# Kernel tuning notes

Measured on AMD Instinct MI355X. Metric: run time of the kernel, lower is better.

## Reference

```python
import jax, jax.numpy as jnp
import numpy as np

B, L, S, D, H, TOPK = 8, 2048, 1000, 1024, 8, 10
E = D // H  # d_keys = 128


def setup_inputs() -> dict:
    key = jax.random.key(0)
    ks = jax.random.split(key, 8)
    s = 1.0 / np.sqrt(D)
    return {
        "target_embedding": jax.random.normal(ks[0], (B, L, D), dtype=jnp.float32),
        "source_embedding": jax.random.normal(ks[1], (S, D), dtype=jnp.float32),
        "Wq": jax.random.normal(ks[2], (D, D), dtype=jnp.float32) * s,
        "bq": jnp.zeros((D,), dtype=jnp.float32),
        "Wk": jax.random.normal(ks[3], (D, D), dtype=jnp.float32) * s,
        "bk": jnp.zeros((D,), dtype=jnp.float32),
        "Wo": jax.random.normal(ks[4], (D, D), dtype=jnp.float32) * s,
        "bo": jnp.zeros((D,), dtype=jnp.float32),
        "data_id": 0,
    }


def reference(target_embedding, source_embedding, Wq, bq, Wk, bk, Wo, bo, data_id):
    # data_id is unused by the original module's math.
    b, l, d = target_embedding.shape
    h, e, topk = H, E, TOPK
    scale = 1.0 / np.sqrt(e)

    q = (target_embedding @ Wq + bq).reshape(b, l, h, e)   # [B,L,H,E]
    k = (source_embedding @ Wk + bk).reshape(-1, h, e)      # [S,H,E]

    scores = jnp.einsum('blhe,she->bhls', q, k)             # [B,H,L,S]
    A = jax.nn.softmax(scale * scores, axis=-1)             # dropout is eval-mode identity
    tmps = A.sum(axis=2)                                    # [B,H,S] head-wise column mass
    _, idxs = jax.lax.top_k(tmps, topk)                     # [B,H,topk]

    kh = jnp.transpose(k, (1, 0, 2))                        # [H,S,E]
    # gather per (batch, head) the topk source key vectors
    tok = kh[jnp.arange(h)[None, :, None], idxs, :]         # [B,H,topk,E]
    tok = jnp.transpose(tok, (0, 2, 1, 3)).reshape(b, topk, h * e)  # [B,topk,D]
    return tok @ Wo + bo                                    # [B,topk,D]
```

## Files before the change

### kernel.cpp

```cpp
#include <hip/hip_runtime.h>
#include <hip/hip_bf16.h>
#include <math.h>

constexpr int B_ = 8;
constexpr int L_ = 2048;
constexpr int S_ = 1000;
constexpr int D_ = 1024;
constexpr int H_ = 8;
constexpr int E_ = 128;
constexpr int TOPK_ = 10;
constexpr float SCALE_LOG2E_ = 0.12751744f;

typedef __attribute__((ext_vector_type(8))) short short8;
typedef __attribute__((ext_vector_type(4))) float f32x4;

__device__ inline unsigned short f2bf(float x) {
    unsigned u = __float_as_uint(x);
    unsigned r = (u + 0x7fffu + ((u >> 16) & 1u)) >> 16;
    return (unsigned short)r;
}
__device__ inline float bf2f(unsigned short s) {
    return __uint_as_float(((unsigned)s) << 16);
}

__device__ __forceinline__ float fexp2(float x) {
#if __has_builtin(__builtin_amdgcn_exp2f)
    return __builtin_amdgcn_exp2f(x);
#else
    return __expf(x * 0.69314718056f);
#endif
}

typedef __attribute__((address_space(1))) const unsigned int gas_u32;
typedef __attribute__((address_space(3))) unsigned int las_u32;
__device__ __forceinline__ void gload_lds16(const void* g, void* l) {
    __builtin_amdgcn_global_load_lds((gas_u32*)g, (las_u32*)l, 16, 0, 0);
}

__global__ __launch_bounds__(256) void gemm_bias_kernel(
    const float* __restrict__ A, const float* __restrict__ Bm,
    const float* __restrict__ bias, float* __restrict__ C,
    int M, int N, int Kd)
{
    __shared__ float As[16][65];
    __shared__ float Bs[16][68];

    const int t  = threadIdx.x;
    const int tx = t & 15;
    const int ty = t >> 4;
    const int m0 = blockIdx.y * 64;
    const int n0 = blockIdx.x * 64;

    float acc[4][4];
#pragma unroll
    for (int i = 0; i < 4; ++i)
#pragma unroll
        for (int j = 0; j < 4; ++j) acc[i][j] = 0.f;

    for (int k0 = 0; k0 < Kd; k0 += 16) {
        {
            const int row = t >> 2;
            const int c4  = (t & 3) * 4;
            float4 v = {0.f, 0.f, 0.f, 0.f};
            if (m0 + row < M)
                v = *(const float4*)&A[(size_t)(m0 + row) * Kd + k0 + c4];
            As[c4 + 0][row] = v.x;
            As[c4 + 1][row] = v.y;
            As[c4 + 2][row] = v.z;
            As[c4 + 3][row] = v.w;
        }
        {
            const int row = t >> 4;
            const int c4  = (t & 15) * 4;
            float4 v = *(const float4*)&Bm[(size_t)(k0 + row) * N + n0 + c4];
            *(float4*)&Bs[row][c4] = v;
        }
        __syncthreads();
#pragma unroll
        for (int k = 0; k < 16; ++k) {
            float a[4], b[4];
#pragma unroll
            for (int i = 0; i < 4; ++i) a[i] = As[k][ty * 4 + i];
            float4 bv = *(const float4*)&Bs[k][tx * 4];
            b[0] = bv.x; b[1] = bv.y; b[2] = bv.z; b[3] = bv.w;
#pragma unroll
            for (int i = 0; i < 4; ++i)
#pragma unroll
                for (int j = 0; j < 4; ++j) acc[i][j] += a[i] * b[j];
        }
        __syncthreads();
    }

#pragma unroll
    for (int i = 0; i < 4; ++i) {
        const int row = m0 + ty * 4 + i;
        if (row < M) {
#pragma unroll
            for (int j = 0; j < 4; ++j) {
                const int col = n0 + tx * 4 + j;
                C[(size_t)row * N + col] = acc[i][j] + bias[col];
            }
        }
    }
}

__global__ __launch_bounds__(256) void splitWT_kernel(
    const float* __restrict__ W,
    unsigned short* __restrict__ WTh, unsigned short* __restrict__ WTl)
{
    __shared__ __attribute__((aligned(16))) float tile[64][68];
    const int t  = threadIdx.x;
    const int k0 = blockIdx.y * 64, n0 = blockIdx.x * 64;
#pragma unroll
    for (int it = 0; it < 4; ++it) {
        int id = it * 256 + t;
        int r = id >> 4, c = id & 15;
        *(float4*)&tile[r][c * 4] = *(const float4*)&W[(size_t)(k0 + r) * D_ + n0 + c * 4];
    }
    __syncthreads();
#pragma unroll
    for (int it = 0; it < 4; ++it) {
        int id = it * 256 + t;
        int n = id >> 4, c = id & 15;
        unsigned short hs[4], ls[4];
#pragma unroll
        for (int i = 0; i < 4; ++i) {
            float x = tile[c * 4 + i][n];
            hs[i] = f2bf(x);
            ls[i] = f2bf(x - bf2f(hs[i]));
        }
        size_t o = (size_t)(n0 + n) * D_ + k0 + c * 4;
        uint2 uh; uh.x = (unsigned)hs[0] | ((unsigned)hs[1] << 16);
                  uh.y = (unsigned)hs[2] | ((unsigned)hs[3] << 16);
        uint2 ul; ul.x = (unsigned)ls[0] | ((unsigned)ls[1] << 16);
                  ul.y = (unsigned)ls[2] | ((unsigned)ls[3] << 16);
        *(uint2*)&WTh[o] = uh;
        *(uint2*)&WTl[o] = ul;
    }
}

__global__ __launch_bounds__(256) void split_src_kernel(
    const float* __restrict__ src,
    unsigned short* __restrict__ Sh, unsigned short* __restrict__ Sl)
{
    int idx  = blockIdx.x * 256 + threadIdx.x;
    int base = idx * 4;
    int row  = base >> 10;
    float4 v = {0.f, 0.f, 0.f, 0.f};
    if (row < S_) v = *(const float4*)&src[base];
    float xs[4] = {v.x, v.y, v.z, v.w};
    unsigned short hs[4], ls[4];
#pragma unroll
    for (int i = 0; i < 4; ++i) {
        hs[i] = f2bf(xs[i]);
        ls[i] = f2bf(xs[i] - bf2f(hs[i]));
    }
    uint2 uh; uh.x = (unsigned)hs[0] | ((unsigned)hs[1] << 16);
              uh.y = (unsigned)hs[2] | ((unsigned)hs[3] << 16);
    uint2 ul; ul.x = (unsigned)ls[0] | ((unsigned)ls[1] << 16);
              ul.y = (unsigned)ls[2] | ((unsigned)ls[3] << 16);
    *(uint2*)&Sh[base] = uh;
    *(uint2*)&Sl[base] = ul;
}

__global__ __launch_bounds__(256, 2) void kproj_kernel(
    const unsigned short* __restrict__ Sh, const unsigned short* __restrict__ Sl,
    const unsigned short* __restrict__ WkTh, const unsigned short* __restrict__ WkTl,
    const float* __restrict__ bk,
    float* __restrict__ Kbuf,
    unsigned short* __restrict__ Kh, unsigned short* __restrict__ Kl)
{
    __shared__ __attribute__((aligned(16))) unsigned short Ah[128 * 64];
    __shared__ __attribute__((aligned(16))) unsigned short Al[128 * 64];
    __shared__ __attribute__((aligned(16))) unsigned short Bh[128 * 64];
    __shared__ __attribute__((aligned(16))) unsigned short Bl[128 * 64];

    const int t    = threadIdx.x;
    const int lane = t & 63, w = t >> 6;
    const int mb   = blockIdx.x >> 3;
    const int n0   = (blockIdx.x & 7) * 128;

    f32x4 acc[2][8];
#pragma unroll
    for (int m = 0; m < 2; ++m)
#pragma unroll
        for (int n = 0; n < 8; ++n) acc[m][n] = (f32x4){0.f, 0.f, 0.f, 0.f};

    for (int k0 = 0; k0 < D_; k0 += 64) {
        __syncthreads();
#pragma unroll
        for (int it = 0; it < 4; ++it) {
            int r = it * 32 + (t >> 3), c = t & 7;
            size_t gofs = (size_t)r * D_ + k0 + ((c ^ (r & 7)) << 3);
            int db = it * 4096 + t * 16;
            gload_lds16(&Sh[(size_t)(mb * 128) * D_ + gofs], (char*)Ah + db);
            gload_lds16(&Sl[(size_t)(mb * 128) * D_ + gofs], (char*)Al + db);
            gload_lds16(&WkTh[(size_t)n0 * D_ + gofs], (char*)Bh + db);
            gload_lds16(&WkTl[(size_t)n0 * D_ + gofs], (char*)Bl + db);
        }
        __syncthreads();

#pragma unroll
        for (int ki = 0; ki < 2; ++ki) {
            short8 ah[2], al[2];
#pragma unroll
            for (int m = 0; m < 2; ++m) {
                int r = w * 32 + m * 16 + (lane & 15);
                int slot = ki * 4 + (lane >> 4);
                int lofs = r * 64 + ((slot ^ (r & 7)) << 3);
                ah[m] = *(short8*)&Ah[lofs];
                al[m] = *(short8*)&Al[lofs];
            }
#pragma unroll
            for (int n = 0; n < 8; ++n) {
                int nn = n * 16 + (lane & 15);
                int slot = ki * 4 + (lane >> 4);
                int lofs = nn * 64 + ((slot ^ (nn & 7)) << 3);
                short8 bh = *(short8*)&Bh[lofs];
                short8 bl = *(short8*)&Bl[lofs];
#pragma unroll
                for (int m = 0; m < 2; ++m) {
                    acc[m][n] = __builtin_amdgcn_mfma_f32_16x16x32_bf16(ah[m], bh, acc[m][n], 0, 0, 0);
                    acc[m][n] = __builtin_amdgcn_mfma_f32_16x16x32_bf16(ah[m], bl, acc[m][n], 0, 0, 0);
                    acc[m][n] = __builtin_amdgcn_mfma_f32_16x16x32_bf16(al[m], bh, acc[m][n], 0, 0, 0);
                }
            }
        }
    }

#pragma unroll
    for (int n = 0; n < 8; ++n) {
        int col = n0 + n * 16 + (lane & 15);
        float bkv = bk[col];
#pragma unroll
        for (int m = 0; m < 2; ++m) {
            int rbase = mb * 128 + w * 32 + m * 16 + ((lane >> 4) << 2);
#pragma unroll
            for (int r = 0; r < 4; ++r) {
                int row = rbase + r;
                unsigned short hh = 0, ll = 0;
                if (row < S_) {
                    float kv = acc[m][n][r] + bkv;
                    Kbuf[(size_t)row * D_ + col] = kv;
                    hh = f2bf(kv);
                    ll = f2bf(kv - bf2f(hh));
                }
                Kh[(size_t)row * D_ + col] = hh;
                Kl[(size_t)row * D_ + col] = ll;
            }
        }
    }
}

__global__ __launch_bounds__(256, 3) void qproj_kernel(
    const float* __restrict__ tgt,
    const unsigned short* __restrict__ WqTh, const unsigned short* __restrict__ WqTl,
    const float* __restrict__ bq,
    unsigned short* __restrict__ qhb, unsigned short* __restrict__ qlb)
{
    __shared__ __attribute__((aligned(16))) unsigned short Bh[2][128 * 32];
    __shared__ __attribute__((aligned(16))) unsigned short Bl[2][128 * 32];

    const int t    = threadIdx.x;
    const int lane = t & 63, w = t >> 6;
    const int x    = blockIdx.x & 7;
    const int jj   = blockIdx.x >> 3;
    const int n0   = (jj & 7) * 128;
    const int mb   = (jj >> 3) * 8 + x;

    f32x4 acc[2][8];
#pragma unroll
    for (int m = 0; m < 2; ++m)
#pragma unroll
        for (int n = 0; n < 8; ++n) acc[m][n] = (f32x4){0.f, 0.f, 0.f, 0.f};

#define QB_ISSUE(KT, BUF)                                                   \
    do {                                                                    \
        _Pragma("unroll")                                                   \
        for (int it = 0; it < 2; ++it) {                                    \
            int id = it * 256 + t;                                          \
            int line = id >> 4, sub = id & 15;                              \
            int gs = sub ^ (line & 15);                                     \
            size_t gb = (size_t)(n0 + line * 4 + (gs >> 2)) * D_            \
                        + (KT) * 32 + ((gs & 3) << 3);                      \
            gload_lds16(&WqTh[gb], (char*)&Bh[(BUF)][0] + id * 16);         \
            gload_lds16(&WqTl[gb], (char*)&Bl[(BUF)][0] + id * 16);         \
        }                                                                   \
    } while (0)

#define QA_LOAD(KT, XA)                                                     \
    do {                                                                    \
        _Pragma("unroll")                                                   \
        for (int m = 0; m < 2; ++m) {                                       \
            int r = mb * 128 + w * 32 + m * 16 + (lane & 15);               \
            const float* ga = &tgt[(size_t)r * D_ + (KT) * 32 + (lane >> 4) * 8]; \
            XA[m][0] = *(const float4*)ga;                                  \
            XA[m][1] = *(const float4*)(ga + 4);                            \
        }                                                                   \
    } while (0)

#define QP_COMPUTE(XA, BUF)                                                 \
    do {                                                                    \
        short8 ah[2], al[2];                                                \
        _Pragma("unroll")                                                   \
        for (int m = 0; m < 2; ++m) {                                       \
            float xs[8] = {XA[m][0].x, XA[m][0].y, XA[m][0].z, XA[m][0].w,  \
                           XA[m][1].x, XA[m][1].y, XA[m][1].z, XA[m][1].w}; \
            _Pragma("unroll")                                               \
            for (int j = 0; j < 8; ++j) {                                   \
                unsigned short hh = f2bf(xs[j]);                            \
                ah[m][j] = (short)hh;                                       \
                al[m][j] = (short)f2bf(xs[j] - bf2f(hh));                   \
            }                                                               \
        }                                                                   \
        _Pragma("unroll")                                                   \
        for (int n = 0; n < 8; ++n) {                                       \
            int nn   = n * 16 + (lane & 15);                                \
            int line = nn >> 2;                                             \
            int sub  = (nn & 3) * 4 + (lane >> 4);                          \
            int lofs = line * 128 + ((sub ^ (line & 15)) << 3);             \
            short8 bh = *(short8*)&Bh[(BUF)][lofs];                         \
            short8 bl = *(short8*)&Bl[(BUF)][lofs];                         \
            _Pragma("unroll")                                               \
            for (int m = 0; m < 2; ++m) {                                   \
                acc[m][n] = __builtin_amdgcn_mfma_f32_16x16x32_bf16(ah[m], bh, acc[m][n], 0, 0, 0); \
                acc[m][n] = __builtin_amdgcn_mfma_f32_16x16x32_bf16(ah[m], bl, acc[m][n], 0, 0, 0); \
                acc[m][n] = __builtin_amdgcn_mfma_f32_16x16x32_bf16(al[m], bh, acc[m][n], 0, 0, 0); \
            }                                                               \
        }                                                                   \
    } while (0)

    float4 xa0[2][2], xa1[2][2];
    QB_ISSUE(0, 0);
    QA_LOAD(0, xa0);

#pragma unroll 1
    for (int kt2 = 0; kt2 < 16; ++kt2) {
        const int kt = kt2 * 2;
        __syncthreads();
        if (kt + 1 < 32) { QB_ISSUE(kt + 1, 1); QA_LOAD(kt + 1, xa1); }
        QP_COMPUTE(xa0, 0);
        __syncthreads();
        if (kt + 2 < 32) { QB_ISSUE(kt + 2, 0); QA_LOAD(kt + 2, xa0); }
        QP_COMPUTE(xa1, 1);
    }
#undef QB_ISSUE
#undef QA_LOAD
#undef QP_COMPUTE

#pragma unroll
    for (int n = 0; n < 8; ++n) {
        int col = n0 + n * 16 + (lane & 15);
        float bqv = bq[col];
#pragma unroll
        for (int m = 0; m < 2; ++m) {
            int rbase = mb * 128 + w * 32 + m * 16 + ((lane >> 4) << 2);
#pragma unroll
            for (int r = 0; r < 4; ++r) {
                float q = (acc[m][n][r] + bqv) * SCALE_LOG2E_;
                unsigned short hh = f2bf(q);
                qhb[(size_t)(rbase + r) * D_ + col] = hh;
                qlb[(size_t)(rbase + r) * D_ + col] = f2bf(q - bf2f(hh));
            }
        }
    }
}

__global__ __launch_bounds__(256, 2) void scores2p_kernel(
    const unsigned short* __restrict__ qhb, const unsigned short* __restrict__ qlb,
    const unsigned short* __restrict__ Kh, const unsigned short* __restrict__ Kl,
    float* __restrict__ tmps, int b0)
{
    __shared__ __attribute__((aligned(16))) unsigned short KB[2][4][32 * 128];
    __shared__ float tmps_l[1024];

    const int t    = threadIdx.x;
    const int lane = t & 63, w = t >> 6;
    const int blk  = blockIdx.x;
    const int bb   = blk >> 6;
    const int h    = (blk >> 3) & 7;
    const int lt   = blk & 7;
    const int qrow0 = bb * L_ + lt * 256;
    const int bh_i  = (b0 + bb) * H_ + h;
    const int kr0   = t >> 4;
    const int kc0   = t & 15;

    for (int i = t; i < 1024; i += 256) tmps_l[i] = 0.f;

#define SC_ISSUE0(ST, BUF)                                                  \
    do {                                                                    \
        _Pragma("unroll")                                                   \
        for (int it = 0; it < 4; ++it) {                                    \
            int r = it * 16 + kr0;                                          \
            size_t g = (size_t)((ST) * 64 + r) * D_ + h * E_                \
                       + ((kc0 ^ (r & 15)) << 3);                           \
            int db = (it & 1) * 4096 + t * 16;                              \
            gload_lds16(&Kh[g], (char*)&KB[(BUF)][it >> 1][0] + db);        \
        }                                                                   \
    } while (0)

#define SC_ISSUE1(ST, BUF)                                                  \
    do {                                                                    \
        _Pragma("unroll")                                                   \
        for (int it = 0; it < 4; ++it) {                                    \
            int r = it * 16 + kr0;                                          \
            size_t g = (size_t)((ST) * 64 + r) * D_ + h * E_                \
                       + ((kc0 ^ (r & 15)) << 3);                           \
            int pl = it >> 1;                                               \
            int db = (it & 1) * 4096 + t * 16;                              \
            gload_lds16(&Kh[g], (char*)&KB[(BUF)][pl][0] + db);             \
            gload_lds16(&Kl[g], (char*)&KB[(BUF)][pl + 2][0] + db);         \
        }                                                                   \
    } while (0)

    SC_ISSUE0(0, 1);

    short8 qh[4][4], ql[4][4];
#pragma unroll
    for (int ch = 0; ch < 8; ++ch) {
        __syncthreads();
#pragma unroll
        for (int it = 0; it < 2; ++it) {
            int r = it * 16 + kr0;
            size_t g = (size_t)(qrow0 + ch * 32 + r) * D_ + h * E_ + kc0 * 8;
            int lofs = r * 128 + ((kc0 ^ (r & 15)) << 3);
            *(uint4*)&KB[0][0][lofs] = *(const uint4*)&qhb[g];
            *(uint4*)&KB[0][1][lofs] = *(const uint4*)&qlb[g];
        }
        __syncthreads();
        if ((ch >> 1) == w) {
#pragma unroll
            for (int j = 0; j < 2; ++j) {
                int rg = (ch & 1) * 2 + j;
#pragma unroll
                for (int ki = 0; ki < 4; ++ki) {
                    int rq = j * 16 + (lane & 15);
                    int slot = ki * 4 + (lane >> 4);
                    int lofs = rq * 128 + ((slot ^ (rq & 15)) << 3);
                    qh[rg][ki] = *(short8*)&KB[0][0][lofs];
                    ql[rg][ki] = *(short8*)&KB[0][1][lofs];
                }
            }
        }
    }

    float zacc[4][4];
#pragma unroll
    for (int rg = 0; rg < 4; ++rg)
#pragma unroll
        for (int r = 0; r < 4; ++r) zacc[rg][r] = 0.f;
    float invZ[4][4];

    int cur = 1;

    for (int u = 0; u < 16; ++u) {
        __syncthreads();
        if (u < 15) SC_ISSUE0(u + 1, cur ^ 1);
        else        SC_ISSUE1(0, cur ^ 1);

#pragma unroll
        for (int nfh = 0; nfh < 2; ++nfh) {
            f32x4 acc[4][2];
#pragma unroll
            for (int rg = 0; rg < 4; ++rg)
#pragma unroll
                for (int n2 = 0; n2 < 2; ++n2) acc[rg][n2] = (f32x4){0.f, 0.f, 0.f, 0.f};

#pragma unroll
            for (int ki = 0; ki < 4; ++ki)
#pragma unroll
                for (int n2 = 0; n2 < 2; ++n2) {
                    int nf = nfh * 2 + n2;
                    int sr = nf * 16 + (lane & 15);
                    int slot = ki * 4 + (lane >> 4);
                    int lofs = (sr & 31) * 128 + ((slot ^ (sr & 15)) << 3);
                    short8 bh = *(short8*)&KB[cur][sr >> 5][lofs];
#pragma unroll
                    for (int rg = 0; rg < 4; ++rg)
                        acc[rg][n2] = __builtin_amdgcn_mfma_f32_16x16x32_bf16(qh[rg][ki], bh, acc[rg][n2], 0, 0, 0);
                }

#pragma unroll
            for (int n2 = 0; n2 < 2; ++n2) {
                int s = u * 64 + (nfh * 2 + n2) * 16 + (lane & 15);
                if (s < S_) {
#pragma unroll
                    for (int rg = 0; rg < 4; ++rg)
#pragma unroll
                        for (int r = 0; r < 4; ++r)
                            zacc[rg][r] += fexp2(acc[rg][n2][r]);
                }
            }
        }

        if (u == 15) {
#pragma unroll
            for (int rg = 0; rg < 4; ++rg)
#pragma unroll
                for (int r = 0; r < 4; ++r) {
                    float z = zacc[rg][r];
                    z += __shfl_xor(z, 1);
                    z += __shfl_xor(z, 2);
                    z += __shfl_xor(z, 4);
                    z += __shfl_xor(z, 8);
                    invZ[rg][r] = 1.f / z;
                }
        }
        cur ^= 1;
    }

    for (int u = 0; u < 16; ++u) {
        __syncthreads();
        if (u < 15) SC_ISSUE1(u + 1, cur ^ 1);

#pragma unroll
        for (int nfh = 0; nfh < 2; ++nfh) {
            f32x4 acc[4][2];
#pragma unroll
            for (int rg = 0; rg < 4; ++rg)
#pragma unroll
                for (int n2 = 0; n2 < 2; ++n2) acc[rg][n2] = (f32x4){0.f, 0.f, 0.f, 0.f};

#pragma unroll
            for (int ki = 0; ki < 4; ++ki)
#pragma unroll
                for (int n2 = 0; n2 < 2; ++n2) {
                    int nf = nfh * 2 + n2;
                    int sr = nf * 16 + (lane & 15);
                    int pl = sr >> 5;
                    int slot = ki * 4 + (lane >> 4);
                    int lofs = (sr & 31) * 128 + ((slot ^ (sr & 15)) << 3);
                    short8 bh = *(short8*)&KB[cur][pl][lofs];
                    short8 bl = *(short8*)&KB[cur][pl + 2][lofs];
#pragma unroll
                    for (int rg = 0; rg < 4; ++rg) {
                        acc[rg][n2] = __builtin_amdgcn_mfma_f32_16x16x32_bf16(qh[rg][ki], bh, acc[rg][n2], 0, 0, 0);
                        acc[rg][n2] = __builtin_amdgcn_mfma_f32_16x16x32_bf16(qh[rg][ki], bl, acc[rg][n2], 0, 0, 0);
                        acc[rg][n2] = __builtin_amdgcn_mfma_f32_16x16x32_bf16(ql[rg][ki], bh, acc[rg][n2], 0, 0, 0);
                    }
                }

#pragma unroll
            for (int n2 = 0; n2 < 2; ++n2) {
                int s = u * 64 + (nfh * 2 + n2) * 16 + (lane & 15);
                if (s < S_) {
                    float val = 0.f;
#pragma unroll
                    for (int rg = 0; rg < 4; ++rg)
#pragma unroll
                        for (int r = 0; r < 4; ++r)
                            val += fexp2(acc[rg][n2][r]) * invZ[rg][r];
                    atomicAdd(&tmps_l[s], val);
                }
            }
        }
        cur ^= 1;
    }
#undef SC_ISSUE0
#undef SC_ISSUE1

    __syncthreads();
    for (int i = t; i < S_; i += 256)
        atomicAdd(&tmps[(size_t)bh_i * S_ + i], tmps_l[i]);
}

__global__ __launch_bounds__(256) void topk_kernel(
    const float* __restrict__ tmps, int* __restrict__ idxs)
{
    const int bh = blockIdx.x;
    const int t  = threadIdx.x;
    __shared__ float v[S_];
    __shared__ float rv[256];
    __shared__ int   ri[256];

    for (int i = t; i < S_; i += 256) v[i] = tmps[(size_t)bh * S_ + i];
    __syncthreads();

    for (int it = 0; it < TOPK_; ++it) {
        float best = -1e38f;
        int bi = 0x7fffffff;
        for (int s = t; s < S_; s += 256) {
            const float x = v[s];
            if (x > best) { best = x; bi = s; }
        }
        rv[t] = best; ri[t] = bi;
        __syncthreads();
        for (int k = 128; k > 0; k >>= 1) {
            if (t < k) {
                const float x = rv[t + k];
                const int  xi = ri[t + k];
                if (x > rv[t] || (x == rv[t] && xi < ri[t])) { rv[t] = x; ri[t] = xi; }
            }
            __syncthreads();
        }
        if (t == 0) {
            idxs[bh * TOPK_ + it] = ri[0];
            v[ri[0]] = -1e38f;
        }
        __syncthreads();
    }
}

__global__ __launch_bounds__(256) void gather_kernel(
    const float* __restrict__ K, const int* __restrict__ idxs,
    float* __restrict__ tok)
{
    const int o = blockIdx.x * 256 + threadIdx.x;
    if (o >= B_ * TOPK_ * D_) return;
    const int d  = o & (D_ - 1);
    const int tt = (o >> 10) % TOPK_;
    const int b  = o / (D_ * TOPK_);
    const int h  = d >> 7;
    const int s  = idxs[(b * H_ + h) * TOPK_ + tt];
    tok[o] = K[(size_t)s * D_ + d];
}

extern "C" void kernel_launch(void* const* d_in, const int* in_sizes, int n_in,
                              void* d_out, int out_size, void* d_ws, size_t ws_size,
                              hipStream_t stream)
{
    const float* tgt = (const float*)d_in[0];
    const float* src = (const float*)d_in[1];
    const float* Wq  = (const float*)d_in[2];
    const float* bq  = (const float*)d_in[3];
    const float* Wk  = (const float*)d_in[4];
    const float* bk  = (const float*)d_in[5];
    const float* Wo  = (const float*)d_in[6];
    const float* bo  = (const float*)d_in[7];
    float* out = (float*)d_out;

    char* ws = (char*)d_ws;
    size_t off = 0;
    float*          Kbuf = (float*)(ws + off);          off += (size_t)S_ * D_ * 4;
    float*          tmps = (float*)(ws + off);          off += (size_t)B_ * H_ * S_ * 4;
    int*            idxs = (int*)(ws + off);            off += (size_t)B_ * H_ * TOPK_ * 4;
    off = (off + 255) & ~(size_t)255;
    float*          tok  = (float*)(ws + off);          off += (size_t)B_ * TOPK_ * D_ * 4;
    unsigned short* Kh   = (unsigned short*)(ws + off); off += (size_t)1024 * D_ * 2;
    unsigned short* Kl   = (unsigned short*)(ws + off); off += (size_t)1024 * D_ * 2;
    unsigned short* WqTh = (unsigned short*)(ws + off); off += (size_t)D_ * D_ * 2;
    unsigned short* WqTl = (unsigned short*)(ws + off); off += (size_t)D_ * D_ * 2;
    unsigned short* WkTh = (unsigned short*)(ws + off); off += (size_t)D_ * D_ * 2;
    unsigned short* WkTl = (unsigned short*)(ws + off); off += (size_t)D_ * D_ * 2;
    unsigned short* Sh   = (unsigned short*)(ws + off); off += (size_t)1024 * D_ * 2;
    unsigned short* Sl   = (unsigned short*)(ws + off); off += (size_t)1024 * D_ * 2;
    unsigned short* planes = (unsigned short*)(ws + off);
    const size_t fixed_bytes = off;
    const size_t plane_elems_per_b = (size_t)L_ * D_;

    int nb_fit = 1;
    if (ws_size > fixed_bytes) {
        size_t f = (ws_size - fixed_bytes) / (2 * plane_elems_per_b * 2);
        nb_fit = (f < 1) ? 1 : (f > 8 ? 8 : (int)f);
    }

    hipMemsetAsync(tmps, 0, (size_t)B_ * H_ * S_ * sizeof(float), stream);

    split_src_kernel<<<(1024 * D_) / (256 * 4), 256, 0, stream>>>(src, Sh, Sl);
    {
        dim3 g(D_ / 64, D_ / 64);
        splitWT_kernel<<<g, 256, 0, stream>>>(Wq, WqTh, WqTl);
        splitWT_kernel<<<g, 256, 0, stream>>>(Wk, WkTh, WkTl);
    }

    kproj_kernel<<<64, 256, 0, stream>>>(Sh, Sl, WkTh, WkTl, bk, Kbuf, Kh, Kl);

    for (int b0 = 0; b0 < B_; b0 += nb_fit) {
        int nb = (B_ - b0 < nb_fit) ? (B_ - b0) : nb_fit;
        unsigned short* qhb = planes;
        unsigned short* qlb = qhb + (size_t)nb_fit * plane_elems_per_b;

        qproj_kernel<<<nb * 128, 256, 0, stream>>>(
            tgt + (size_t)b0 * L_ * D_, WqTh, WqTl, bq, qhb, qlb);
        scores2p_kernel<<<nb * 64, 256, 0, stream>>>(qhb, qlb, Kh, Kl, tmps, b0);
    }

    topk_kernel<<<B_ * H_, 256, 0, stream>>>(tmps, idxs);
    gather_kernel<<<(B_ * TOPK_ * D_ + 255) / 256, 256, 0, stream>>>(Kbuf, idxs, tok);
    {
        dim3 g(D_ / 64, (B_ * TOPK_ + 63) / 64);
        gemm_bias_kernel<<<g, 256, 0, stream>>>(tok, Wo, bo, out, B_ * TOPK_, D_, D_);
    }
}
```

Before: 385.9 us.

## Fuse Q projection into scores kernel, keeping per-head Q tile on-chip

Merges qproj_kernel and scores2p_kernel into one kernel in which each block computes the 256x128 Q tile for its (batch, head, L-tile) and passes it through LDS straight into registers for the softmax column-sum pass. This drops the bf16 hi/lo Q planes written to and re-read from global memory, the workspace batching loop and one launch per batch chunk. In exchange the accumulator tile doubles (4x8 MFMA tiles per wave), which raises register pressure, and the A-operand global loads are no longer prefetched one step ahead.

```diff
diff --git a/kernel.cpp b/kernel.cpp
--- a/kernel.cpp
+++ b/kernel.cpp
@@ -252,140 +252,150 @@
     }
 }
 
-__global__ __launch_bounds__(256, 3) void qproj_kernel(
+__global__ __launch_bounds__(256, 2) void fused_qs_kernel(
     const float* __restrict__ tgt,
     const unsigned short* __restrict__ WqTh, const unsigned short* __restrict__ WqTl,
     const float* __restrict__ bq,
-    unsigned short* __restrict__ qhb, unsigned short* __restrict__ qlb)
-{
-    __shared__ __attribute__((aligned(16))) unsigned short Bh[2][128 * 32];
-    __shared__ __attribute__((aligned(16))) unsigned short Bl[2][128 * 32];
+    const unsigned short* __restrict__ Kh, const unsigned short* __restrict__ Kl,
+    float* __restrict__ tmps)
+{
+    __shared__ __attribute__((aligned(16))) unsigned short KB[2][4][32 * 128];
+    __shared__ float tmps_l[1024];
 
     const int t    = threadIdx.x;
     const int lane = t & 63, w = t >> 6;
-    const int x    = blockIdx.x & 7;
-    const int jj   = blockIdx.x >> 3;
-    const int n0   = (jj & 7) * 128;
-    const int mb   = (jj >> 3) * 8 + x;
-
-    f32x4 acc[2][8];
-#pragma unroll
-    for (int m = 0; m < 2; ++m)
+    const int blk  = blockIdx.x;
+    const int lt   = blk & 7;
+    const int h    = (blk >> 3) & 7;
+    const int b    = blk >> 6;
+    const int qrow0 = b * L_ + lt * 256;
+    const int bh_i  = b * H_ + h;
+    const int n0w   = h * E_;
+    const int kr0   = t >> 4;
+    const int kc0   = t & 15;
+
+    for (int i = t; i < 1024; i += 256) tmps_l[i] = 0.f;
+
+    f32x4 acc[4][8];
+#pragma unroll
+    for (int m = 0; m < 4; ++m)
 #pragma unroll
         for (int n = 0; n < 8; ++n) acc[m][n] = (f32x4){0.f, 0.f, 0.f, 0.f};
 
-#define QB_ISSUE(KT, BUF)                                                   \
+#define FB_ISSUE(KT, BH, BL)                                                \
     do {                                                                    \
         _Pragma("unroll")                                                   \
         for (int it = 0; it < 2; ++it) {                                    \
             int id = it * 256 + t;                                          \
             int line = id >> 4, sub = id & 15;                              \
             int gs = sub ^ (line & 15);                                     \
-            size_t gb = (size_t)(n0 + line * 4 + (gs >> 2)) * D_            \
+            size_t gb = (size_t)(n0w + line * 4 + (gs >> 2)) * D_           \
                         + (KT) * 32 + ((gs & 3) << 3);                      \
-            gload_lds16(&WqTh[gb], (char*)&Bh[(BUF)][0] + id * 16);         \
-            gload_lds16(&WqTl[gb], (char*)&Bl[(BUF)][0] + id * 16);         \
+            gload_lds16(&WqTh[gb], (char*)(BH) + id * 16);                  \
+            gload_lds16(&WqTl[gb], (char*)(BL) + id * 16);                  \
         }                                                                   \
     } while (0)
 
-#define QA_LOAD(KT, XA)                                                     \
-    do {                                                                    \
-        _Pragma("unroll")                                                   \
-        for (int m = 0; m < 2; ++m) {                                       \
-            int r = mb * 128 + w * 32 + m * 16 + (lane & 15);               \
-            const float* ga = &tgt[(size_t)r * D_ + (KT) * 32 + (lane >> 4) * 8]; \
-            XA[m][0] = *(const float4*)ga;                                  \
-            XA[m][1] = *(const float4*)(ga + 4);                            \
-        }                                                                   \
-    } while (0)
-
-#define QP_COMPUTE(XA, BUF)                                                 \
-    do {                                                                    \
-        short8 ah[2], al[2];                                                \
-        _Pragma("unroll")                                                   \
-        for (int m = 0; m < 2; ++m) {                                       \
-            float xs[8] = {XA[m][0].x, XA[m][0].y, XA[m][0].z, XA[m][0].w,  \
-                           XA[m][1].x, XA[m][1].y, XA[m][1].z, XA[m][1].w}; \
-            _Pragma("unroll")                                               \
-            for (int j = 0; j < 8; ++j) {                                   \
-                unsigned short hh = f2bf(xs[j]);                            \
-                ah[m][j] = (short)hh;                                       \
-                al[m][j] = (short)f2bf(xs[j] - bf2f(hh));                   \
-            }                                                               \
-        }                                                                   \
-        _Pragma("unroll")                                                   \
-        for (int n = 0; n < 8; ++n) {                                       \
-            int nn   = n * 16 + (lane & 15);                                \
-            int line = nn >> 2;                                             \
-            int sub  = (nn & 3) * 4 + (lane >> 4);                          \
-            int lofs = line * 128 + ((sub ^ (line & 15)) << 3);             \
-            short8 bh = *(short8*)&Bh[(BUF)][lofs];                         \
-            short8 bl = *(short8*)&Bl[(BUF)][lofs];                         \
-            _Pragma("unroll")                                               \
-            for (int m = 0; m < 2; ++m) {                                   \
-                acc[m][n] = __builtin_amdgcn_mfma_f32_16x16x32_bf16(ah[m], bh, acc[m][n], 0, 0, 0); \
-                acc[m][n] = __builtin_amdgcn_mfma_f32_16x16x32_bf16(ah[m], bl, acc[m][n], 0, 0, 0); \
-                acc[m][n] = __builtin_amdgcn_mfma_f32_16x16x32_bf16(al[m], bh, acc[m][n], 0, 0, 0); \
-            }                                                               \
-        }                                                                   \
-    } while (0)
-
-    float4 xa0[2][2], xa1[2][2];
-    QB_ISSUE(0, 0);
-    QA_LOAD(0, xa0);
-
+    {
+        unsigned short* Bh0 = &KB[0][0][0];
+        unsigned short* Bh1 = &KB[0][1][0];
+        unsigned short* Bl0 = &KB[0][2][0];
+        unsigned short* Bl1 = &KB[0][3][0];
+
+        FB_ISSUE(0, Bh0, Bl0);
 #pragma unroll 1
-    for (int kt2 = 0; kt2 < 16; ++kt2) {
-        const int kt = kt2 * 2;
-        __syncthreads();
-        if (kt + 1 < 32) { QB_ISSUE(kt + 1, 1); QA_LOAD(kt + 1, xa1); }
-        QP_COMPUTE(xa0, 0);
-        __syncthreads();
-        if (kt + 2 < 32) { QB_ISSUE(kt + 2, 0); QA_LOAD(kt + 2, xa0); }
-        QP_COMPUTE(xa1, 1);
-    }
-#undef QB_ISSUE
-#undef QA_LOAD
-#undef QP_COMPUTE
-
-#pragma unroll
-    for (int n = 0; n < 8; ++n) {
-        int col = n0 + n * 16 + (lane & 15);
-        float bqv = bq[col];
-#pragma unroll
-        for (int m = 0; m < 2; ++m) {
-            int rbase = mb * 128 + w * 32 + m * 16 + ((lane >> 4) << 2);
+        for (int kt = 0; kt < 32; ++kt) {
+            const int cur = kt & 1;
+            __syncthreads();
+            if (kt < 31) FB_ISSUE(kt + 1, cur ? Bh0 : Bh1, cur ? Bl0 : Bl1);
+
+            short8 ah[4], al[4];
+#pragma unroll
+            for (int m = 0; m < 4; ++m) {
+                int r = qrow0 + w * 64 + m * 16 + (lane & 15);
+                const float* ga = &tgt[(size_t)r * D_ + kt * 32 + (lane >> 4) * 8];
+                float4 x0 = *(const float4*)ga;
+                float4 x1 = *(const float4*)(ga + 4);
+                float xs[8] = {x0.x, x0.y, x0.z, x0.w, x1.x, x1.y, x1.z, x1.w};
+#pragma unroll
+                for (int j = 0; j < 8; ++j) {
+                    unsigned short hh = f2bf(xs[j]);
+                    ah[m][j] = (short)hh;
+                    al[m][j] = (short)f2bf(xs[j] - bf2f(hh));
+                }
+            }
+            unsigned short* BH = cur ? Bh1 : Bh0;
+            unsigned short* BL = cur ? Bl1 : Bl0;
+#pragma unroll
+            for (int n = 0; n < 8; ++n) {
+                int nn   = n * 16 + (lane & 15);
+                int line = nn >> 2;
+                int sub  = (nn & 3) * 4 + (lane >> 4);
+                int lofs = line * 128 + ((sub ^ (line & 15)) << 3);
+                short8 bh = *(short8*)&BH[lofs];
+                short8 bl = *(short8*)&BL[lofs];
+#pragma unroll
+                for (int m = 0; m < 4; ++m) {
+                    acc[m][n] = __builtin_amdgcn_mfma_f32_16x16x32_bf16(ah[m], bh, acc[m][n], 0, 0, 0);
+                    acc[m][n] = __builtin_amdgcn_mfma_f32_16x16x32_bf16(ah[m], bl, acc[m][n], 0, 0, 0);
+                    acc[m][n] = __builtin_amdgcn_mfma_f32_16x16x32_bf16(al[m], bh, acc[m][n], 0, 0, 0);
+                }
+            }
+        }
+    }
+#undef FB_ISSUE
+
+    float bqv[8];
+#pragma unroll
+    for (int n = 0; n < 8; ++n) bqv[n] = bq[n0w + n * 16 + (lane & 15)];
+
+    unsigned short* P = &KB[0][0][0];
+    short8 qh[4][4], ql[4][4];
+
+    __syncthreads();
+#pragma unroll
+    for (int m = 0; m < 4; ++m)
+#pragma unroll
+        for (int n = 0; n < 8; ++n)
 #pragma unroll
             for (int r = 0; r < 4; ++r) {
-                float q = (acc[m][n][r] + bqv) * SCALE_LOG2E_;
-                unsigned short hh = f2bf(q);
-                qhb[(size_t)(rbase + r) * D_ + col] = hh;
-                qlb[(size_t)(rbase + r) * D_ + col] = f2bf(q - bf2f(hh));
-            }
-        }
-    }
-}
-
-__global__ __launch_bounds__(256, 2) void scores2p_kernel(
-    const unsigned short* __restrict__ qhb, const unsigned short* __restrict__ qlb,
-    const unsigned short* __restrict__ Kh, const unsigned short* __restrict__ Kl,
-    float* __restrict__ tmps, int b0)
-{
-    __shared__ __attribute__((aligned(16))) unsigned short KB[2][4][32 * 128];
-    __shared__ float tmps_l[1024];
-
-    const int t    = threadIdx.x;
-    const int lane = t & 63, w = t >> 6;
-    const int blk  = blockIdx.x;
-    const int bb   = blk >> 6;
-    const int h    = (blk >> 3) & 7;
-    const int lt   = blk & 7;
-    const int qrow0 = bb * L_ + lt * 256;
-    const int bh_i  = (b0 + bb) * H_ + h;
-    const int kr0   = t >> 4;
-    const int kc0   = t & 15;
-
-    for (int i = t; i < 1024; i += 256) tmps_l[i] = 0.f;
+                int R = w * 64 + m * 16 + ((lane >> 4) << 2) + r;
+                int c = n * 16 + (lane & 15);
+                float qv = (acc[m][n][r] + bqv[n]) * SCALE_LOG2E_;
+                P[(R >> 5) * 4096 + (R & 31) * 128 +
+                  (((c >> 3) ^ (R & 15)) << 3) + (c & 7)] = f2bf(qv);
+            }
+    __syncthreads();
+#pragma unroll
+    for (int rg = 0; rg < 4; ++rg)
+#pragma unroll
+        for (int ki = 0; ki < 4; ++ki)
+            qh[rg][ki] = *(short8*)&P[(w * 2 + (rg >> 1)) * 4096 +
+                ((rg & 1) * 16 + (lane & 15)) * 128 +
+                (((ki * 4 + (lane >> 4)) ^ (lane & 15)) << 3)];
+    __syncthreads();
+#pragma unroll
+    for (int m = 0; m < 4; ++m)
+#pragma unroll
+        for (int n = 0; n < 8; ++n)
+#pragma unroll
+            for (int r = 0; r < 4; ++r) {
+                int R = w * 64 + m * 16 + ((lane >> 4) << 2) + r;
+                int c = n * 16 + (lane & 15);
+                float qv = (acc[m][n][r] + bqv[n]) * SCALE_LOG2E_;
+                unsigned short hh = f2bf(qv);
+                P[(R >> 5) * 4096 + (R & 31) * 128 +
+                  (((c >> 3) ^ (R & 15)) << 3) + (c & 7)] = f2bf(qv - bf2f(hh));
+            }
+    __syncthreads();
+#pragma unroll
+    for (int rg = 0; rg < 4; ++rg)
+#pragma unroll
+        for (int ki = 0; ki < 4; ++ki)
+            ql[rg][ki] = *(short8*)&P[(w * 2 + (rg >> 1)) * 4096 +
+                ((rg & 1) * 16 + (lane & 15)) * 128 +
+                (((ki * 4 + (lane >> 4)) ^ (lane & 15)) << 3)];
+    __syncthreads();
 
 #define SC_ISSUE0(ST, BUF)                                                  \
     do {                                                                    \
@@ -415,35 +425,6 @@
 
     SC_ISSUE0(0, 1);
 
-    short8 qh[4][4], ql[4][4];
-#pragma unroll
-    for (int ch = 0; ch < 8; ++ch) {
-        __syncthreads();
-#pragma unroll
-        for (int it = 0; it < 2; ++it) {
-            int r = it * 16 + kr0;
-            size_t g = (size_t)(qrow0 + ch * 32 + r) * D_ + h * E_ + kc0 * 8;
-            int lofs = r * 128 + ((kc0 ^ (r & 15)) << 3);
-            *(uint4*)&KB[0][0][lofs] = *(const uint4*)&qhb[g];
-            *(uint4*)&KB[0][1][lofs] = *(const uint4*)&qlb[g];
-        }
-        __syncthreads();
-        if ((ch >> 1) == w) {
-#pragma unroll
-            for (int j = 0; j < 2; ++j) {
-                int rg = (ch & 1) * 2 + j;
-#pragma unroll
-                for (int ki = 0; ki < 4; ++ki) {
-                    int rq = j * 16 + (lane & 15);
-                    int slot = ki * 4 + (lane >> 4);
-                    int lofs = rq * 128 + ((slot ^ (rq & 15)) << 3);
-                    qh[rg][ki] = *(short8*)&KB[0][0][lofs];
-                    ql[rg][ki] = *(short8*)&KB[0][1][lofs];
-                }
-            }
-        }
-    }
-
     float zacc[4][4];
 #pragma unroll
     for (int rg = 0; rg < 4; ++rg)
@@ -460,11 +441,11 @@
 
 #pragma unroll
         for (int nfh = 0; nfh < 2; ++nfh) {
-            f32x4 acc[4][2];
+            f32x4 sacc[4][2];
 #pragma unroll
             for (int rg = 0; rg < 4; ++rg)
 #pragma unroll
-                for (int n2 = 0; n2 < 2; ++n2) acc[rg][n2] = (f32x4){0.f, 0.f, 0.f, 0.f};
+                for (int n2 = 0; n2 < 2; ++n2) sacc[rg][n2] = (f32x4){0.f, 0.f, 0.f, 0.f};
 
 #pragma unroll
             for (int ki = 0; ki < 4; ++ki)
@@ -477,7 +458,7 @@
                     short8 bh = *(short8*)&KB[cur][sr >> 5][lofs];
 #pragma unroll
                     for (int rg = 0; rg < 4; ++rg)
-                        acc[rg][n2] = __builtin_amdgcn_mfma_f32_16x16x32_bf16(qh[rg][ki], bh, acc[rg][n2], 0, 0, 0);
+                        sacc[rg][n2] = __builtin_amdgcn_mfma_f32_16x16x32_bf16(qh[rg][ki], bh, sacc[rg][n2], 0, 0, 0);
                 }
 
 #pragma unroll
@@ -488,7 +469,7 @@
                     for (int rg = 0; rg < 4; ++rg)
 #pragma unroll
                         for (int r = 0; r < 4; ++r)
-                            zacc[rg][r] += fexp2(acc[rg][n2][r]);
+                            zacc[rg][r] += fexp2(sacc[rg][n2][r]);
                 }
             }
         }
@@ -515,11 +496,11 @@
 
 #pragma unroll
         for (int nfh = 0; nfh < 2; ++nfh) {
-            f32x4 acc[4][2];
+            f32x4 sacc[4][2];
 #pragma unroll
             for (int rg = 0; rg < 4; ++rg)
 #pragma unroll
-                for (int n2 = 0; n2 < 2; ++n2) acc[rg][n2] = (f32x4){0.f, 0.f, 0.f, 0.f};
+                for (int n2 = 0; n2 < 2; ++n2) sacc[rg][n2] = (f32x4){0.f, 0.f, 0.f, 0.f};
 
 #pragma unroll
             for (int ki = 0; ki < 4; ++ki)
@@ -534,9 +515,9 @@
                     short8 bl = *(short8*)&KB[cur][pl + 2][lofs];
 #pragma unroll
                     for (int rg = 0; rg < 4; ++rg) {
-                        acc[rg][n2] = __builtin_amdgcn_mfma_f32_16x16x32_bf16(qh[rg][ki], bh, acc[rg][n2], 0, 0, 0);
-                        acc[rg][n2] = __builtin_amdgcn_mfma_f32_16x16x32_bf16(qh[rg][ki], bl, acc[rg][n2], 0, 0, 0);
-                        acc[rg][n2] = __builtin_amdgcn_mfma_f32_16x16x32_bf16(ql[rg][ki], bh, acc[rg][n2], 0, 0, 0);
+                        sacc[rg][n2] = __builtin_amdgcn_mfma_f32_16x16x32_bf16(qh[rg][ki], bh, sacc[rg][n2], 0, 0, 0);
+                        sacc[rg][n2] = __builtin_amdgcn_mfma_f32_16x16x32_bf16(qh[rg][ki], bl, sacc[rg][n2], 0, 0, 0);
+                        sacc[rg][n2] = __builtin_amdgcn_mfma_f32_16x16x32_bf16(ql[rg][ki], bh, sacc[rg][n2], 0, 0, 0);
                     }
                 }
 
@@ -549,7 +530,7 @@
                     for (int rg = 0; rg < 4; ++rg)
 #pragma unroll
                         for (int r = 0; r < 4; ++r)
-                            val += fexp2(acc[rg][n2][r]) * invZ[rg][r];
+                            val += fexp2(sacc[rg][n2][r]) * invZ[rg][r];
                     atomicAdd(&tmps_l[s], val);
                 }
             }
@@ -644,15 +625,6 @@
     unsigned short* WkTl = (unsigned short*)(ws + off); off += (size_t)D_ * D_ * 2;
     unsigned short* Sh   = (unsigned short*)(ws + off); off += (size_t)1024 * D_ * 2;
     unsigned short* Sl   = (unsigned short*)(ws + off); off += (size_t)1024 * D_ * 2;
-    unsigned short* planes = (unsigned short*)(ws + off);
-    const size_t fixed_bytes = off;
-    const size_t plane_elems_per_b = (size_t)L_ * D_;
-
-    int nb_fit = 1;
-    if (ws_size > fixed_bytes) {
-        size_t f = (ws_size - fixed_bytes) / (2 * plane_elems_per_b * 2);
-        nb_fit = (f < 1) ? 1 : (f > 8 ? 8 : (int)f);
-    }
 
     hipMemsetAsync(tmps, 0, (size_t)B_ * H_ * S_ * sizeof(float), stream);
 
@@ -665,15 +637,8 @@
 
     kproj_kernel<<<64, 256, 0, stream>>>(Sh, Sl, WkTh, WkTl, bk, Kbuf, Kh, Kl);
 
-    for (int b0 = 0; b0 < B_; b0 += nb_fit) {
-        int nb = (B_ - b0 < nb_fit) ? (B_ - b0) : nb_fit;
-        unsigned short* qhb = planes;
-        unsigned short* qlb = qhb + (size_t)nb_fit * plane_elems_per_b;
-
-        qproj_kernel<<<nb * 128, 256, 0, stream>>>(
-            tgt + (size_t)b0 * L_ * D_, WqTh, WqTl, bq, qhb, qlb);
-        scores2p_kernel<<<nb * 64, 256, 0, stream>>>(qhb, qlb, Kh, Kl, tmps, b0);
-    }
+    fused_qs_kernel<<<B_ * H_ * 8, 256, 0, stream>>>(
+        tgt, WqTh, WqTl, bq, Kh, Kl, tmps);
 
     topk_kernel<<<B_ * H_, 256, 0, stream>>>(tmps, idxs);
     gather_kernel<<<(B_ * TOPK_ * D_ + 255) / 256, 256, 0, stream>>>(Kbuf, idxs, tok);
```

New measurement: 418.4 us. 8.4% more time.

## Fuse gather into output GEMM, source split into kproj, merge weight splits

Applied to the files above, without the earlier changes.

Three small kernels are folded into their neighbours. The top-k gather now happens inside the output GEMM's A-tile load. The source bf16 hi/lo split is done in registers inside kproj from fp32 global loads, instead of a separate pass staged through LDS. The two weight-split launches become one launch with a z dimension. This removes launches and intermediate buffers, but kproj now reads fp32 source directly and converts it per wave, which may cost more global traffic and ALU work there.

```diff
diff --git a/kernel.cpp b/kernel.cpp
--- a/kernel.cpp
+++ b/kernel.cpp
@@ -37,10 +37,10 @@
     __builtin_amdgcn_global_load_lds((gas_u32*)g, (las_u32*)l, 16, 0, 0);
 }
 
-__global__ __launch_bounds__(256) void gemm_bias_kernel(
-    const float* __restrict__ A, const float* __restrict__ Bm,
-    const float* __restrict__ bias, float* __restrict__ C,
-    int M, int N, int Kd)
+__global__ __launch_bounds__(256) void gemm_gather_bias_kernel(
+    const float* __restrict__ Kbuf, const int* __restrict__ idxs,
+    const float* __restrict__ Bm, const float* __restrict__ bias,
+    float* __restrict__ C, int M, int N)
 {
     __shared__ float As[16][65];
     __shared__ float Bs[16][68];
@@ -57,17 +57,22 @@
 #pragma unroll
         for (int j = 0; j < 4; ++j) acc[i][j] = 0.f;
 
-    for (int k0 = 0; k0 < Kd; k0 += 16) {
+    for (int k0 = 0; k0 < D_; k0 += 16) {
         {
-            const int row = t >> 2;
-            const int c4  = (t & 3) * 4;
+            const int row = m0 + (t >> 2);
+            const int k   = k0 + (t & 3) * 4;
             float4 v = {0.f, 0.f, 0.f, 0.f};
-            if (m0 + row < M)
-                v = *(const float4*)&A[(size_t)(m0 + row) * Kd + k0 + c4];
-            As[c4 + 0][row] = v.x;
-            As[c4 + 1][row] = v.y;
-            As[c4 + 2][row] = v.z;
-            As[c4 + 3][row] = v.w;
+            if (row < M) {
+                int b  = row / TOPK_;
+                int tt = row - b * TOPK_;
+                int s  = idxs[(b * H_ + (k >> 7)) * TOPK_ + tt];
+                v = *(const float4*)&Kbuf[(size_t)s * D_ + k];
+            }
+            const int rr = t >> 2, c4 = (t & 3) * 4;
+            As[c4 + 0][rr] = v.x;
+            As[c4 + 1][rr] = v.y;
+            As[c4 + 2][rr] = v.z;
+            As[c4 + 3][rr] = v.w;
         }
         {
             const int row = t >> 4;
@@ -104,10 +109,15 @@
     }
 }
 
-__global__ __launch_bounds__(256) void splitWT_kernel(
-    const float* __restrict__ W,
-    unsigned short* __restrict__ WTh, unsigned short* __restrict__ WTl)
+__global__ __launch_bounds__(256) void splitWT2_kernel(
+    const float* __restrict__ Wq, const float* __restrict__ Wk,
+    unsigned short* __restrict__ WqTh, unsigned short* __restrict__ WqTl,
+    unsigned short* __restrict__ WkTh, unsigned short* __restrict__ WkTl)
 {
+    const float* W = (blockIdx.z == 0) ? Wq : Wk;
+    unsigned short* WTh = (blockIdx.z == 0) ? WqTh : WkTh;
+    unsigned short* WTl = (blockIdx.z == 0) ? WqTl : WkTl;
+
     __shared__ __attribute__((aligned(16))) float tile[64][68];
     const int t  = threadIdx.x;
     const int k0 = blockIdx.y * 64, n0 = blockIdx.x * 64;
@@ -139,39 +149,13 @@
     }
 }
 
-__global__ __launch_bounds__(256) void split_src_kernel(
+__global__ __launch_bounds__(256, 2) void kproj_kernel(
     const float* __restrict__ src,
-    unsigned short* __restrict__ Sh, unsigned short* __restrict__ Sl)
-{
-    int idx  = blockIdx.x * 256 + threadIdx.x;
-    int base = idx * 4;
-    int row  = base >> 10;
-    float4 v = {0.f, 0.f, 0.f, 0.f};
-    if (row < S_) v = *(const float4*)&src[base];
-    float xs[4] = {v.x, v.y, v.z, v.w};
-    unsigned short hs[4], ls[4];
-#pragma unroll
-    for (int i = 0; i < 4; ++i) {
-        hs[i] = f2bf(xs[i]);
-        ls[i] = f2bf(xs[i] - bf2f(hs[i]));
-    }
-    uint2 uh; uh.x = (unsigned)hs[0] | ((unsigned)hs[1] << 16);
-              uh.y = (unsigned)hs[2] | ((unsigned)hs[3] << 16);
-    uint2 ul; ul.x = (unsigned)ls[0] | ((unsigned)ls[1] << 16);
-              ul.y = (unsigned)ls[2] | ((unsigned)ls[3] << 16);
-    *(uint2*)&Sh[base] = uh;
-    *(uint2*)&Sl[base] = ul;
-}
-
-__global__ __launch_bounds__(256, 2) void kproj_kernel(
-    const unsigned short* __restrict__ Sh, const unsigned short* __restrict__ Sl,
     const unsigned short* __restrict__ WkTh, const unsigned short* __restrict__ WkTl,
     const float* __restrict__ bk,
     float* __restrict__ Kbuf,
     unsigned short* __restrict__ Kh, unsigned short* __restrict__ Kl)
 {
-    __shared__ __attribute__((aligned(16))) unsigned short Ah[128 * 64];
-    __shared__ __attribute__((aligned(16))) unsigned short Al[128 * 64];
     __shared__ __attribute__((aligned(16))) unsigned short Bh[128 * 64];
     __shared__ __attribute__((aligned(16))) unsigned short Bl[128 * 64];
 
@@ -193,8 +177,6 @@
             int r = it * 32 + (t >> 3), c = t & 7;
             size_t gofs = (size_t)r * D_ + k0 + ((c ^ (r & 7)) << 3);
             int db = it * 4096 + t * 16;
-            gload_lds16(&Sh[(size_t)(mb * 128) * D_ + gofs], (char*)Ah + db);
-            gload_lds16(&Sl[(size_t)(mb * 128) * D_ + gofs], (char*)Al + db);
             gload_lds16(&WkTh[(size_t)n0 * D_ + gofs], (char*)Bh + db);
             gload_lds16(&WkTl[(size_t)n0 * D_ + gofs], (char*)Bl + db);
         }
@@ -205,11 +187,20 @@
             short8 ah[2], al[2];
 #pragma unroll
             for (int m = 0; m < 2; ++m) {
-                int r = w * 32 + m * 16 + (lane & 15);
-                int slot = ki * 4 + (lane >> 4);
-                int lofs = r * 64 + ((slot ^ (r & 7)) << 3);
-                ah[m] = *(short8*)&Ah[lofs];
-                al[m] = *(short8*)&Al[lofs];
+                int r = mb * 128 + w * 32 + m * 16 + (lane & 15);
+                float4 x0 = {0.f, 0.f, 0.f, 0.f}, x1 = {0.f, 0.f, 0.f, 0.f};
+                if (r < S_) {
+                    const float* ga = &src[(size_t)r * D_ + k0 + (ki * 4 + (lane >> 4)) * 8];
+                    x0 = *(const float4*)ga;
+                    x1 = *(const float4*)(ga + 4);
+                }
+                float xs[8] = {x0.x, x0.y, x0.z, x0.w, x1.x, x1.y, x1.z, x1.w};
+#pragma unroll
+                for (int j = 0; j < 8; ++j) {
+                    unsigned short hh = f2bf(xs[j]);
+                    ah[m][j] = (short)hh;
+                    al[m][j] = (short)f2bf(xs[j] - bf2f(hh));
+                }
             }
 #pragma unroll
             for (int n = 0; n < 8; ++n) {
@@ -601,20 +592,6 @@
     }
 }
 
-__global__ __launch_bounds__(256) void gather_kernel(
-    const float* __restrict__ K, const int* __restrict__ idxs,
-    float* __restrict__ tok)
-{
-    const int o = blockIdx.x * 256 + threadIdx.x;
-    if (o >= B_ * TOPK_ * D_) return;
-    const int d  = o & (D_ - 1);
-    const int tt = (o >> 10) % TOPK_;
-    const int b  = o / (D_ * TOPK_);
-    const int h  = d >> 7;
-    const int s  = idxs[(b * H_ + h) * TOPK_ + tt];
-    tok[o] = K[(size_t)s * D_ + d];
-}
-
 extern "C" void kernel_launch(void* const* d_in, const int* in_sizes, int n_in,
                               void* d_out, int out_size, void* d_ws, size_t ws_size,
                               hipStream_t stream)
@@ -635,15 +612,12 @@
     float*          tmps = (float*)(ws + off);          off += (size_t)B_ * H_ * S_ * 4;
     int*            idxs = (int*)(ws + off);            off += (size_t)B_ * H_ * TOPK_ * 4;
     off = (off + 255) & ~(size_t)255;
-    float*          tok  = (float*)(ws + off);          off += (size_t)B_ * TOPK_ * D_ * 4;
     unsigned short* Kh   = (unsigned short*)(ws + off); off += (size_t)1024 * D_ * 2;
     unsigned short* Kl   = (unsigned short*)(ws + off); off += (size_t)1024 * D_ * 2;
     unsigned short* WqTh = (unsigned short*)(ws + off); off += (size_t)D_ * D_ * 2;
     unsigned short* WqTl = (unsigned short*)(ws + off); off += (size_t)D_ * D_ * 2;
     unsigned short* WkTh = (unsigned short*)(ws + off); off += (size_t)D_ * D_ * 2;
     unsigned short* WkTl = (unsigned short*)(ws + off); off += (size_t)D_ * D_ * 2;
-    unsigned short* Sh   = (unsigned short*)(ws + off); off += (size_t)1024 * D_ * 2;
-    unsigned short* Sl   = (unsigned short*)(ws + off); off += (size_t)1024 * D_ * 2;
     unsigned short* planes = (unsigned short*)(ws + off);
     const size_t fixed_bytes = off;
     const size_t plane_elems_per_b = (size_t)L_ * D_;
@@ -656,14 +630,12 @@
 
     hipMemsetAsync(tmps, 0, (size_t)B_ * H_ * S_ * sizeof(float), stream);
 
-    split_src_kernel<<<(1024 * D_) / (256 * 4), 256, 0, stream>>>(src, Sh, Sl);
     {
-        dim3 g(D_ / 64, D_ / 64);
-        splitWT_kernel<<<g, 256, 0, stream>>>(Wq, WqTh, WqTl);
-        splitWT_kernel<<<g, 256, 0, stream>>>(Wk, WkTh, WkTl);
-    }
-
-    kproj_kernel<<<64, 256, 0, stream>>>(Sh, Sl, WkTh, WkTl, bk, Kbuf, Kh, Kl);
+        dim3 g(D_ / 64, D_ / 64, 2);
+        splitWT2_kernel<<<g, 256, 0, stream>>>(Wq, Wk, WqTh, WqTl, WkTh, WkTl);
+    }
+
+    kproj_kernel<<<64, 256, 0, stream>>>(src, WkTh, WkTl, bk, Kbuf, Kh, Kl);
 
     for (int b0 = 0; b0 < B_; b0 += nb_fit) {
         int nb = (B_ - b0 < nb_fit) ? (B_ - b0) : nb_fit;
@@ -676,9 +648,10 @@
     }
 
     topk_kernel<<<B_ * H_, 256, 0, stream>>>(tmps, idxs);
-    gather_kernel<<<(B_ * TOPK_ * D_ + 255) / 256, 256, 0, stream>>>(Kbuf, idxs, tok);
+
     {
         dim3 g(D_ / 64, (B_ * TOPK_ + 63) / 64);
-        gemm_bias_kernel<<<g, 256, 0, stream>>>(tok, Wo, bo, out, B_ * TOPK_, D_, D_);
-    }
-}
+        gemm_gather_bias_kernel<<<g, 256, 0, stream>>>(
+            Kbuf, idxs, Wo, bo, out, B_ * TOPK_, D_);
+    }
+}
```

Measured after the change: 412.6 us. 1.07x slower.
